# Performance work log

Measured on AMD Instinct MI355X. Metric: run time of the kernel, lower is better.

Reference implementation:

```python
import jax, jax.numpy as jnp
import numpy as np

N_NODES = 100000
N_EDGES = 3200000
NUM_FEATURES = 512
HIDDEN = 16
NUM_CLASSES = 32


def _gcn_conv(x, src, dst, norm, W, b, n):
    # PyG GCNConv: linear transform first, then normalized scatter-add aggregation
    xw = x @ W                          # [N, out]
    msg = xw[src] * norm[:, None]       # gather over edges (incl. self-loops)
    agg = jax.ops.segment_sum(msg, dst, num_segments=n)
    return agg + b


def setup_inputs() -> dict:
    key = jax.random.key(0)
    k_x, k_e, k_w1, k_w2 = jax.random.split(key, 4)
    x = jax.random.normal(k_x, (N_NODES, NUM_FEATURES), dtype=jnp.float32)
    edge_index = jax.random.randint(k_e, (2, N_EDGES), 0, N_NODES, dtype=jnp.int64)
    # Glorot-style init for the two GCNConv weights; zero bias (PyG default)
    W1 = jax.random.normal(k_w1, (NUM_FEATURES, HIDDEN), dtype=jnp.float32) * (1.0 / np.sqrt(NUM_FEATURES))
    b1 = jnp.zeros((HIDDEN,), dtype=jnp.float32)
    W2 = jax.random.normal(k_w2, (HIDDEN, NUM_CLASSES), dtype=jnp.float32) * (1.0 / np.sqrt(HIDDEN))
    b2 = jnp.zeros((NUM_CLASSES,), dtype=jnp.float32)
    return {"x": x, "edge_index": edge_index, "W1": W1, "b1": b1, "W2": W2, "b2": b2}


def reference(x, edge_index, W1, b1, W2, b2):
    n = x.shape[0]
    # add self-loops (PyG GCNConv default add_self_loops=True)
    loops = jnp.arange(n, dtype=edge_index.dtype)
    src = jnp.concatenate([edge_index[0], loops])
    dst = jnp.concatenate([edge_index[1], loops])
    # symmetric normalization D^{-1/2} (A+I) D^{-1/2}
    deg = jax.ops.segment_sum(jnp.ones_like(dst, dtype=x.dtype), dst, num_segments=n)
    dinv = jnp.where(deg > 0, jax.lax.rsqrt(deg), 0.0)
    norm = dinv[src] * dinv[dst]        # [E + N]

    h = jax.nn.relu(_gcn_conv(x, src, dst, norm, W1, b1, n))
    # F.dropout(p=0.5, training=self.training): eval mode -> identity
    out = _gcn_conv(h, src, dst, norm, W2, b2, n)
    return (out, h)
```

## Files before the change

### kernel.cpp

```cpp
#include <hip/hip_runtime.h>
#include <hip/hip_fp16.h>


#define NN 100000
#define NE 3200000
#define FIN 512
#define HID 16
#define NCLS 32
#define NB 391
#define NBP 512
#define CAP_B 9216

#define OFF_BCNT  0
#define OFF_SC    (NBP)
#define OFF_DINV  (NBP + 2*NN)
#define OFF_EP    (NBP + 3*NN)
#define OFF_XWS   (OFF_EP + NB*CAP_B)
#define OFF_HSC   (OFF_XWS + NN*8)

__global__ __launch_bounds__(512) void k_binA(const int* __restrict__ src,
                                              const int* __restrict__ dst,
                                              int* __restrict__ bcnt,
                                              unsigned* __restrict__ ep) {
    __shared__ int hist[NBP];
    __shared__ int gpos[NBP];
    int tid = threadIdx.x;
    hist[tid] = 0;
    __syncthreads();
    int base = blockIdx.x * 4096;
    unsigned rec[8];
    int meta[8];
#pragma unroll
    for (int k = 0; k < 8; ++k) {
        int e = base + tid + k * 512;
        if (e < NE) {
            int s = __builtin_nontemporal_load(src + e);
            int d = __builtin_nontemporal_load(dst + e);
            int b = d >> 8;
            int p = atomicAdd(&hist[b], 1);
            rec[k] = ((unsigned)s << 8) | (unsigned)(d & 255);
            meta[k] = (p << 9) | b;
        } else meta[k] = -1;
    }
    __syncthreads();
    int v = hist[tid];
    if (v > 0) gpos[tid] = atomicAdd(&bcnt[tid], v);
    __syncthreads();
#pragma unroll
    for (int k = 0; k < 8; ++k) {
        if (meta[k] >= 0) {
            int b = meta[k] & 511;
            int p = meta[k] >> 9;
            ep[b * CAP_B + gpos[b] + p] = rec[k];
        }
    }
}

__global__ __launch_bounds__(256) void k_binB(unsigned* __restrict__ ep,
                                              const int* __restrict__ bcnt,
                                              int2* __restrict__ sc,
                                              float* __restrict__ dinv) {
    __shared__ int nh[256];
    __shared__ int ns[256];
    __shared__ int np_[256];
    __shared__ int esL[CAP_B];
    int tid = threadIdx.x;
    int b = blockIdx.x;
    int gbase = b * CAP_B;
    int bc = bcnt[b];
    if (bc > CAP_B) bc = CAP_B;
    nh[tid] = 0;
    __syncthreads();
    for (int t = tid; t < bc; t += 256)
        atomicAdd(&nh[ep[gbase + t] & 255], 1);
    __syncthreads();
    int v = nh[tid];
    ns[tid] = v;
    __syncthreads();
#pragma unroll
    for (int o = 1; o < 256; o <<= 1) {
        int u = (tid >= o) ? ns[tid - o] : 0;
        __syncthreads();
        ns[tid] += u;
        __syncthreads();
    }
    int ex = ns[tid] - v;
    np_[tid] = ex;
    __syncthreads();
    for (int t = tid; t < bc; t += 256) {
        unsigned r = ep[gbase + t];
        int dl = r & 255;
        int p = atomicAdd(&np_[dl], 1);
        esL[p] = (int)(r >> 8);
    }
    __syncthreads();
    for (int t = tid; t < bc; t += 256)
        ep[gbase + t] = (unsigned)esL[t];
    int node = b * 256 + tid;
    if (node < NN) {
        sc[node] = make_int2(gbase + ex, v);
        dinv[node] = rsqrtf((float)(v + 1));
    }
}

__global__ __launch_bounds__(256) void k_xw(const float* __restrict__ x,
                                            const float* __restrict__ W1,
                                            const float* __restrict__ dinv,
                                            __half* __restrict__ xws) {
    __shared__ float w1[FIN * HID];
    for (int t = threadIdx.x; t < FIN * HID; t += 256) {
        int k = t >> 4, j = t & 15;
        int s = (k * 4 + ((j >> 2) ^ ((k >> 2) & 3))) * 4 + (j & 3);
        w1[s] = W1[t];
    }
    __syncthreads();
    int w  = threadIdx.x >> 6;
    int nl = (threadIdx.x >> 2) & 15;
    int c  = threadIdx.x & 3;
    int n0 = blockIdx.x * 128 + w * 32 + nl;
    int n1 = n0 + 16;
    bool v0 = n0 < NN, v1 = n1 < NN;
    const float4* x4 = reinterpret_cast<const float4*>(x);
    const float4* r0 = x4 + (v0 ? (size_t)n0 * (FIN / 4) : 0);
    const float4* r1 = x4 + (v1 ? (size_t)n1 * (FIN / 4) : 0);
    const float4* wv = reinterpret_cast<const float4*>(w1);
    float a0[HID], a1[HID];
#pragma unroll
    for (int j = 0; j < HID; ++j) { a0[j] = 0.f; a1[j] = 0.f; }
#pragma unroll 4
    for (int t = 0; t < 32; ++t) {
        int qk = c + 4 * t;
        float4 xv0 = r0[qk];
        float4 xv1 = r1[qk];
        const float4* wb = wv + qk * 16;
#pragma unroll
        for (int e = 0; e < 4; ++e) {
            float xe0 = (e == 0) ? xv0.x : (e == 1) ? xv0.y : (e == 2) ? xv0.z : xv0.w;
            float xe1 = (e == 0) ? xv1.x : (e == 1) ? xv1.y : (e == 2) ? xv1.z : xv1.w;
#pragma unroll
            for (int j4 = 0; j4 < 4; ++j4) {
                float4 w4 = wb[e * 4 + (j4 ^ c)];
                a0[j4 * 4 + 0] += xe0 * w4.x;
                a0[j4 * 4 + 1] += xe0 * w4.y;
                a0[j4 * 4 + 2] += xe0 * w4.z;
                a0[j4 * 4 + 3] += xe0 * w4.w;
                a1[j4 * 4 + 0] += xe1 * w4.x;
                a1[j4 * 4 + 1] += xe1 * w4.y;
                a1[j4 * 4 + 2] += xe1 * w4.z;
                a1[j4 * 4 + 3] += xe1 * w4.w;
            }
        }
    }
#pragma unroll
    for (int j = 0; j < HID; ++j) {
        a0[j] += __shfl_xor(a0[j], 1);
        a0[j] += __shfl_xor(a0[j], 2);
        a1[j] += __shfl_xor(a1[j], 1);
        a1[j] += __shfl_xor(a1[j], 2);
    }
    if (c == 0) {
        if (v0) {
            float dv = dinv[n0];
            __half2 hv[8];
#pragma unroll
            for (int k = 0; k < 8; ++k)
                hv[k] = __floats2half2_rn(a0[2 * k] * dv, a0[2 * k + 1] * dv);
            float4* o = reinterpret_cast<float4*>(xws + (size_t)n0 * HID);
            o[0] = *reinterpret_cast<float4*>(&hv[0]);
            o[1] = *reinterpret_cast<float4*>(&hv[4]);
        }
        if (v1) {
            float dv = dinv[n1];
            __half2 hv[8];
#pragma unroll
            for (int k = 0; k < 8; ++k)
                hv[k] = __floats2half2_rn(a1[2 * k] * dv, a1[2 * k + 1] * dv);
            float4* o = reinterpret_cast<float4*>(xws + (size_t)n1 * HID);
            o[0] = *reinterpret_cast<float4*>(&hv[0]);
            o[1] = *reinterpret_cast<float4*>(&hv[4]);
        }
    }
}

__global__ __launch_bounds__(256) void k_gather1(const int2* __restrict__ sc,
                                                 const int* __restrict__ esrc,
                                                 const __half2* __restrict__ xws2,
                                                 const float* __restrict__ dinv,
                                                 const float* __restrict__ b1,
                                                 float* __restrict__ hout,
                                                 __half2* __restrict__ hsc2) {
    int wave = (blockIdx.x * 256 + threadIdx.x) >> 6;
    if (wave >= NN) return;
    int i = wave;
    int lane = threadIdx.x & 63;
    int j2 = lane & 7;
    int c = lane >> 3;
    int2 s2 = sc[i];
    int st = s2.x, en = st + s2.y;
    float sx[8], sy[8];
#pragma unroll
    for (int k = 0; k < 8; ++k) { sx[k] = 0.f; sy[k] = 0.f; }
    for (int e = st + c; e < en; e += 64) {
        int a[8];
#pragma unroll
        for (int k = 0; k < 8; ++k) {
            int ee = e + 8 * k;
            a[k] = __builtin_nontemporal_load(esrc + (ee < en ? ee : e));
        }
#pragma unroll
        for (int k = 0; k < 8; ++k) {
            float2 f = __half22float2(xws2[a[k] * 8 + j2]);
            bool ok = (e + 8 * k) < en;
            sx[k] += ok ? f.x : 0.f;
            sy[k] += ok ? f.y : 0.f;
        }
    }
    float sumx = ((sx[0] + sx[1]) + (sx[2] + sx[3])) + ((sx[4] + sx[5]) + (sx[6] + sx[7]));
    float sumy = ((sy[0] + sy[1]) + (sy[2] + sy[3])) + ((sy[4] + sy[5]) + (sy[6] + sy[7]));
    sumx += __shfl_xor(sumx, 8);  sumy += __shfl_xor(sumy, 8);
    sumx += __shfl_xor(sumx, 16); sumy += __shfl_xor(sumy, 16);
    sumx += __shfl_xor(sumx, 32); sumy += __shfl_xor(sumy, 32);
    if (c == 0) {
        float dv = dinv[i];
        float2 self = __half22float2(xws2[i * 8 + j2]);
        float vx = b1[2 * j2]     + dv * (sumx + self.x);
        float vy = b1[2 * j2 + 1] + dv * (sumy + self.y);
        float hx = vx > 0.f ? vx : 0.f;
        float hy = vy > 0.f ? vy : 0.f;
        *reinterpret_cast<float2*>(hout + i * HID + 2 * j2) = make_float2(hx, hy);
        hsc2[i * 8 + j2] = __floats2half2_rn(hx * dv, hy * dv);
    }
}

__global__ __launch_bounds__(256) void k_gather2h(const int2* __restrict__ sc,
                                                  const int* __restrict__ esrc,
                                                  const __half2* __restrict__ hsc2,
                                                  const float* __restrict__ dinv,
                                                  const float* __restrict__ W2,
                                                  const float* __restrict__ b2,
                                                  float* __restrict__ out) {
    __shared__ float w2s[HID * NCLS];
    __shared__ float b2s[NCLS];
    for (int t = threadIdx.x; t < HID * NCLS; t += 256) w2s[t] = W2[t];
    if (threadIdx.x < NCLS) b2s[threadIdx.x] = b2[threadIdx.x];
    __syncthreads();
    int wave = (blockIdx.x * 256 + threadIdx.x) >> 6;
    if (wave >= NN) return;
    int i = wave;
    int lane = threadIdx.x & 63;
    int j2 = lane & 7;
    int c = lane >> 3;
    int2 s2 = sc[i];
    int st = s2.x, en = st + s2.y;
    float sx[8], sy[8];
#pragma unroll
    for (int k = 0; k < 8; ++k) { sx[k] = 0.f; sy[k] = 0.f; }
    for (int e = st + c; e < en; e += 64) {
        int a[8];
#pragma unroll
        for (int k = 0; k < 8; ++k) {
            int ee = e + 8 * k;
            a[k] = __builtin_nontemporal_load(esrc + (ee < en ? ee : e));
        }
#pragma unroll
        for (int k = 0; k < 8; ++k) {
            float2 f = __half22float2(hsc2[a[k] * 8 + j2]);
            bool ok = (e + 8 * k) < en;
            sx[k] += ok ? f.x : 0.f;
            sy[k] += ok ? f.y : 0.f;
        }
    }
    float sumx = ((sx[0] + sx[1]) + (sx[2] + sx[3])) + ((sx[4] + sx[5]) + (sx[6] + sx[7]));
    float sumy = ((sy[0] + sy[1]) + (sy[2] + sy[3])) + ((sy[4] + sy[5]) + (sy[6] + sy[7]));
    sumx += __shfl_xor(sumx, 8);  sumy += __shfl_xor(sumy, 8);
    sumx += __shfl_xor(sumx, 16); sumy += __shfl_xor(sumy, 16);
    sumx += __shfl_xor(sumx, 32); sumy += __shfl_xor(sumy, 32);
    {
        float2 self = __half22float2(hsc2[i * 8 + j2]);
        sumx += self.x;
        sumy += self.y;
    }
    int jo = lane & 31;
    float acc = 0.f;
#pragma unroll
    for (int p = 0; p < 8; ++p) {
        acc += __shfl(sumx, p) * w2s[(2 * p) * NCLS + jo];
        acc += __shfl(sumy, p) * w2s[(2 * p + 1) * NCLS + jo];
    }
    if (lane < 32)
        out[i * NCLS + jo] = b2s[jo] + dinv[i] * acc;
}

extern "C" void kernel_launch(void* const* d_in, const int* in_sizes, int n_in,
                              void* d_out, int out_size, void* d_ws, size_t ws_size,
                              hipStream_t stream) {
    const float* x  = (const float*)d_in[0];
    const int* ei   = (const int*)d_in[1];
    const float* W1 = (const float*)d_in[2];
    const float* b1 = (const float*)d_in[3];
    const float* W2 = (const float*)d_in[4];
    const float* b2 = (const float*)d_in[5];

    const int* src = ei;
    const int* dst = ei + NE;

    int* wsi = (int*)d_ws;
    int*      bcnt  = wsi + OFF_BCNT;
    int2*     sc    = (int2*)(wsi + OFF_SC);
    float*    dinv  = (float*)(wsi + OFF_DINV);
    unsigned* ep    = (unsigned*)(wsi + OFF_EP);
    __half*   xws   = (__half*)(wsi + OFF_XWS);
    __half2*  xws2  = (__half2*)(wsi + OFF_XWS);
    __half2*  hsc2  = (__half2*)(wsi + OFF_HSC);

    float* outp = (float*)d_out;
    float* hout = outp + NN * NCLS;

    const int B = 256;

    hipMemsetAsync(bcnt, 0, NBP * sizeof(int), stream);
    hipLaunchKernelGGL(k_binA,  dim3((NE + 4095) / 4096), dim3(512), 0, stream, src, dst, bcnt, ep);
    hipLaunchKernelGGL(k_binB,  dim3(NB), dim3(B), 0, stream, ep, bcnt, sc, dinv);
    hipLaunchKernelGGL(k_xw,    dim3((NN + 127) / 128), dim3(B), 0, stream, x, W1, dinv, xws);
    hipLaunchKernelGGL(k_gather1, dim3((NN * 64 + B - 1) / B), dim3(B), 0, stream,
                       sc, (const int*)ep, xws2, dinv, b1, hout, hsc2);
    hipLaunchKernelGGL(k_gather2h, dim3((NN * 64 + B - 1) / B), dim3(B), 0, stream,
                       sc, (const int*)ep, hsc2, dinv, W2, b2, outp);
}
```

Baseline: 193.3 us.

## Process two nodes per wave in both gather kernels to raise memory parallelism

Each wave in the two aggregation kernels now handles two nodes (i and i+N/2). The first 64-edge chunk of both nodes is loaded and gathered together, so more independent loads are in flight per wave, and the remaining chunks are handled in separate loops. The launch grid is halved. The edge-bin scatter store in the binning kernel is switched to a nontemporal store. Costs are higher register pressure and therefore lower occupancy, and there is an odd hsc2==nullptr check in the gather1 tail loop.

```diff
diff --git a/kernel.cpp b/kernel.cpp
--- a/kernel.cpp
+++ b/kernel.cpp
@@ -3,6 +3,7 @@
 
 
 #define NN 100000
+#define NHALF 50000
 #define NE 3200000
 #define FIN 512
 #define HID 16
@@ -51,7 +52,7 @@
         if (meta[k] >= 0) {
             int b = meta[k] & 511;
             int p = meta[k] >> 9;
-            ep[b * CAP_B + gpos[b] + p] = rec[k];
+            __builtin_nontemporal_store(rec[k], &ep[b * CAP_B + gpos[b] + p]);
         }
     }
 }
@@ -189,46 +190,91 @@
                                                  const float* __restrict__ b1,
                                                  float* __restrict__ hout,
                                                  __half2* __restrict__ hsc2) {
-    int wave = (blockIdx.x * 256 + threadIdx.x) >> 6;
-    if (wave >= NN) return;
-    int i = wave;
+    int wv = (blockIdx.x * 256 + threadIdx.x) >> 6;
+    if (wv >= NHALF) return;
+    int i0 = wv, i1 = wv + NHALF;
     int lane = threadIdx.x & 63;
     int j2 = lane & 7;
     int c = lane >> 3;
-    int2 s2 = sc[i];
-    int st = s2.x, en = st + s2.y;
-    float sx[8], sy[8];
-#pragma unroll
-    for (int k = 0; k < 8; ++k) { sx[k] = 0.f; sy[k] = 0.f; }
-    for (int e = st + c; e < en; e += 64) {
+    int2 A = sc[i0], B = sc[i1];
+    int stA = A.x + c, enA = A.x + A.y;
+    int stB = B.x + c, enB = B.x + B.y;
+    float sxA[8], syA[8], sxB[8], syB[8];
+#pragma unroll
+    for (int k = 0; k < 8; ++k) { sxA[k] = 0.f; syA[k] = 0.f; sxB[k] = 0.f; syB[k] = 0.f; }
+    {
+        int aA[8], aB[8];
+#pragma unroll
+        for (int k = 0; k < 8; ++k) {
+            int eA = stA + 8 * k;
+            int eB = stB + 8 * k;
+            aA[k] = __builtin_nontemporal_load(esrc + (eA < enA ? eA : A.x));
+            aB[k] = __builtin_nontemporal_load(esrc + (eB < enB ? eB : B.x));
+        }
+#pragma unroll
+        for (int k = 0; k < 8; ++k) {
+            bool okA = (stA + 8 * k) < enA;
+            bool okB = (stB + 8 * k) < enB;
+            float2 fA = __half22float2(xws2[(okA ? aA[k] : 0) * 8 + j2]);
+            float2 fB = __half22float2(xws2[(okB ? aB[k] : 0) * 8 + j2]);
+            sxA[k] += okA ? fA.x : 0.f;  syA[k] += okA ? fA.y : 0.f;
+            sxB[k] += okB ? fB.x : 0.f;  syB[k] += okB ? fB.y : 0.f;
+        }
+    }
+    for (int e = stA + 64; e < enA; e += 64) {
         int a[8];
 #pragma unroll
         for (int k = 0; k < 8; ++k) {
             int ee = e + 8 * k;
-            a[k] = __builtin_nontemporal_load(esrc + (ee < en ? ee : e));
+            a[k] = __builtin_nontemporal_load(esrc + (ee < enA ? ee : e));
         }
 #pragma unroll
         for (int k = 0; k < 8; ++k) {
             float2 f = __half22float2(xws2[a[k] * 8 + j2]);
-            bool ok = (e + 8 * k) < en;
-            sx[k] += ok ? f.x : 0.f;
-            sy[k] += ok ? f.y : 0.f;
-        }
-    }
-    float sumx = ((sx[0] + sx[1]) + (sx[2] + sx[3])) + ((sx[4] + sx[5]) + (sx[6] + sx[7]));
-    float sumy = ((sy[0] + sy[1]) + (sy[2] + sy[3])) + ((sy[4] + sy[5]) + (sy[6] + sy[7]));
-    sumx += __shfl_xor(sumx, 8);  sumy += __shfl_xor(sumy, 8);
-    sumx += __shfl_xor(sumx, 16); sumy += __shfl_xor(sumy, 16);
-    sumx += __shfl_xor(sumx, 32); sumy += __shfl_xor(sumy, 32);
+            bool ok = (e + 8 * k) < enA;
+            sxA[k] += ok ? f.x : 0.f;
+            syA[k] += ok ? f.y : 0.f;
+        }
+    }
+    for (int e = stB + 64; e < enB; e += 64) {
+        int a[8];
+#pragma unroll
+        for (int k = 0; k < 8; ++k) {
+            int ee = e + 8 * k;
+            a[k] = __builtin_nontemporal_load(esrc + (ee < enB ? ee : e));
+        }
+#pragma unroll
+        for (int k = 0; k < 8; ++k) {
+            float2 f = __half22float2(hsc2 == nullptr ? make_half2(__float2half(0.f), __float2half(0.f)) : xws2[a[k] * 8 + j2]);
+            bool ok = (e + 8 * k) < enB;
+            sxB[k] += ok ? f.x : 0.f;
+            syB[k] += ok ? f.y : 0.f;
+        }
+    }
+    float sumxA = ((sxA[0] + sxA[1]) + (sxA[2] + sxA[3])) + ((sxA[4] + sxA[5]) + (sxA[6] + sxA[7]));
+    float sumyA = ((syA[0] + syA[1]) + (syA[2] + syA[3])) + ((syA[4] + syA[5]) + (syA[6] + syA[7]));
+    float sumxB = ((sxB[0] + sxB[1]) + (sxB[2] + sxB[3])) + ((sxB[4] + sxB[5]) + (sxB[6] + sxB[7]));
+    float sumyB = ((syB[0] + syB[1]) + (syB[2] + syB[3])) + ((syB[4] + syB[5]) + (syB[6] + syB[7]));
+    sumxA += __shfl_xor(sumxA, 8);  sumyA += __shfl_xor(sumyA, 8);
+    sumxA += __shfl_xor(sumxA, 16); sumyA += __shfl_xor(sumyA, 16);
+    sumxA += __shfl_xor(sumxA, 32); sumyA += __shfl_xor(sumyA, 32);
+    sumxB += __shfl_xor(sumxB, 8);  sumyB += __shfl_xor(sumyB, 8);
+    sumxB += __shfl_xor(sumxB, 16); sumyB += __shfl_xor(sumyB, 16);
+    sumxB += __shfl_xor(sumxB, 32); sumyB += __shfl_xor(sumyB, 32);
     if (c == 0) {
-        float dv = dinv[i];
-        float2 self = __half22float2(xws2[i * 8 + j2]);
-        float vx = b1[2 * j2]     + dv * (sumx + self.x);
-        float vy = b1[2 * j2 + 1] + dv * (sumy + self.y);
-        float hx = vx > 0.f ? vx : 0.f;
-        float hy = vy > 0.f ? vy : 0.f;
-        *reinterpret_cast<float2*>(hout + i * HID + 2 * j2) = make_float2(hx, hy);
-        hsc2[i * 8 + j2] = __floats2half2_rn(hx * dv, hy * dv);
+        float dvA = dinv[i0], dvB = dinv[i1];
+        float2 selfA = __half22float2(xws2[i0 * 8 + j2]);
+        float2 selfB = __half22float2(xws2[i1 * 8 + j2]);
+        float vxA = b1[2 * j2]     + dvA * (sumxA + selfA.x);
+        float vyA = b1[2 * j2 + 1] + dvA * (sumyA + selfA.y);
+        float vxB = b1[2 * j2]     + dvB * (sumxB + selfB.x);
+        float vyB = b1[2 * j2 + 1] + dvB * (sumyB + selfB.y);
+        float hxA = vxA > 0.f ? vxA : 0.f, hyA = vyA > 0.f ? vyA : 0.f;
+        float hxB = vxB > 0.f ? vxB : 0.f, hyB = vyB > 0.f ? vyB : 0.f;
+        *reinterpret_cast<float2*>(hout + i0 * HID + 2 * j2) = make_float2(hxA, hyA);
+        *reinterpret_cast<float2*>(hout + i1 * HID + 2 * j2) = make_float2(hxB, hyB);
+        hsc2[i0 * 8 + j2] = __floats2half2_rn(hxA * dvA, hyA * dvA);
+        hsc2[i1 * 8 + j2] = __floats2half2_rn(hxB * dvB, hyB * dvB);
     }
 }
 
@@ -244,51 +290,96 @@
     for (int t = threadIdx.x; t < HID * NCLS; t += 256) w2s[t] = W2[t];
     if (threadIdx.x < NCLS) b2s[threadIdx.x] = b2[threadIdx.x];
     __syncthreads();
-    int wave = (blockIdx.x * 256 + threadIdx.x) >> 6;
-    if (wave >= NN) return;
-    int i = wave;
+    int wv = (blockIdx.x * 256 + threadIdx.x) >> 6;
+    if (wv >= NHALF) return;
+    int i0 = wv, i1 = wv + NHALF;
     int lane = threadIdx.x & 63;
     int j2 = lane & 7;
     int c = lane >> 3;
-    int2 s2 = sc[i];
-    int st = s2.x, en = st + s2.y;
-    float sx[8], sy[8];
-#pragma unroll
-    for (int k = 0; k < 8; ++k) { sx[k] = 0.f; sy[k] = 0.f; }
-    for (int e = st + c; e < en; e += 64) {
+    int2 A = sc[i0], B = sc[i1];
+    int stA = A.x + c, enA = A.x + A.y;
+    int stB = B.x + c, enB = B.x + B.y;
+    float sxA[8], syA[8], sxB[8], syB[8];
+#pragma unroll
+    for (int k = 0; k < 8; ++k) { sxA[k] = 0.f; syA[k] = 0.f; sxB[k] = 0.f; syB[k] = 0.f; }
+    {
+        int aA[8], aB[8];
+#pragma unroll
+        for (int k = 0; k < 8; ++k) {
+            int eA = stA + 8 * k;
+            int eB = stB + 8 * k;
+            aA[k] = __builtin_nontemporal_load(esrc + (eA < enA ? eA : A.x));
+            aB[k] = __builtin_nontemporal_load(esrc + (eB < enB ? eB : B.x));
+        }
+#pragma unroll
+        for (int k = 0; k < 8; ++k) {
+            bool okA = (stA + 8 * k) < enA;
+            bool okB = (stB + 8 * k) < enB;
+            float2 fA = __half22float2(hsc2[(okA ? aA[k] : 0) * 8 + j2]);
+            float2 fB = __half22float2(hsc2[(okB ? aB[k] : 0) * 8 + j2]);
+            sxA[k] += okA ? fA.x : 0.f;  syA[k] += okA ? fA.y : 0.f;
+            sxB[k] += okB ? fB.x : 0.f;  syB[k] += okB ? fB.y : 0.f;
+        }
+    }
+    for (int e = stA + 64; e < enA; e += 64) {
         int a[8];
 #pragma unroll
         for (int k = 0; k < 8; ++k) {
             int ee = e + 8 * k;
-            a[k] = __builtin_nontemporal_load(esrc + (ee < en ? ee : e));
+            a[k] = __builtin_nontemporal_load(esrc + (ee < enA ? ee : e));
         }
 #pragma unroll
         for (int k = 0; k < 8; ++k) {
             float2 f = __half22float2(hsc2[a[k] * 8 + j2]);
-            bool ok = (e + 8 * k) < en;
-            sx[k] += ok ? f.x : 0.f;
-            sy[k] += ok ? f.y : 0.f;
-        }
-    }
-    float sumx = ((sx[0] + sx[1]) + (sx[2] + sx[3])) + ((sx[4] + sx[5]) + (sx[6] + sx[7]));
-    float sumy = ((sy[0] + sy[1]) + (sy[2] + sy[3])) + ((sy[4] + sy[5]) + (sy[6] + sy[7]));
-    sumx += __shfl_xor(sumx, 8);  sumy += __shfl_xor(sumy, 8);
-    sumx += __shfl_xor(sumx, 16); sumy += __shfl_xor(sumy, 16);
-    sumx += __shfl_xor(sumx, 32); sumy += __shfl_xor(sumy, 32);
+            bool ok = (e + 8 * k) < enA;
+            sxA[k] += ok ? f.x : 0.f;
+            syA[k] += ok ? f.y : 0.f;
+        }
+    }
+    for (int e = stB + 64; e < enB; e += 64) {
+        int a[8];
+#pragma unroll
+        for (int k = 0; k < 8; ++k) {
+            int ee = e + 8 * k;
+            a[k] = __builtin_nontemporal_load(esrc + (ee < enB ? ee : e));
+        }
+#pragma unroll
+        for (int k = 0; k < 8; ++k) {
+            float2 f = __half22float2(hsc2[a[k] * 8 + j2]);
+            bool ok = (e + 8 * k) < enB;
+            sxB[k] += ok ? f.x : 0.f;
+            syB[k] += ok ? f.y : 0.f;
+        }
+    }
+    float sumxA = ((sxA[0] + sxA[1]) + (sxA[2] + sxA[3])) + ((sxA[4] + sxA[5]) + (sxA[6] + sxA[7]));
+    float sumyA = ((syA[0] + syA[1]) + (syA[2] + syA[3])) + ((syA[4] + syA[5]) + (syA[6] + syA[7]));
+    float sumxB = ((sxB[0] + sxB[1]) + (sxB[2] + sxB[3])) + ((sxB[4] + sxB[5]) + (sxB[6] + sxB[7]));
+    float sumyB = ((syB[0] + syB[1]) + (syB[2] + syB[3])) + ((syB[4] + syB[5]) + (syB[6] + syB[7]));
+    sumxA += __shfl_xor(sumxA, 8);  sumyA += __shfl_xor(sumyA, 8);
+    sumxA += __shfl_xor(sumxA, 16); sumyA += __shfl_xor(sumyA, 16);
+    sumxA += __shfl_xor(sumxA, 32); sumyA += __shfl_xor(sumyA, 32);
+    sumxB += __shfl_xor(sumxB, 8);  sumyB += __shfl_xor(sumyB, 8);
+    sumxB += __shfl_xor(sumxB, 16); sumyB += __shfl_xor(sumyB, 16);
+    sumxB += __shfl_xor(sumxB, 32); sumyB += __shfl_xor(sumyB, 32);
     {
-        float2 self = __half22float2(hsc2[i * 8 + j2]);
-        sumx += self.x;
-        sumy += self.y;
+        float2 sA = __half22float2(hsc2[i0 * 8 + j2]);
+        float2 sB = __half22float2(hsc2[i1 * 8 + j2]);
+        sumxA += sA.x;  sumyA += sA.y;
+        sumxB += sB.x;  sumyB += sB.y;
     }
     int jo = lane & 31;
-    float acc = 0.f;
+    float accA = 0.f, accB = 0.f;
 #pragma unroll
     for (int p = 0; p < 8; ++p) {
-        acc += __shfl(sumx, p) * w2s[(2 * p) * NCLS + jo];
-        acc += __shfl(sumy, p) * w2s[(2 * p + 1) * NCLS + jo];
-    }
-    if (lane < 32)
-        out[i * NCLS + jo] = b2s[jo] + dinv[i] * acc;
+        float wx = w2s[(2 * p) * NCLS + jo];
+        float wy = w2s[(2 * p + 1) * NCLS + jo];
+        accA += __shfl(sumxA, p) * wx + __shfl(sumyA, p) * wy;
+        accB += __shfl(sumxB, p) * wx + __shfl(sumyB, p) * wy;
+    }
+    if (lane < 32) {
+        out[i0 * NCLS + jo] = b2s[jo] + dinv[i0] * accA;
+        out[i1 * NCLS + jo] = b2s[jo] + dinv[i1] * accB;
+    }
 }
 
 extern "C" void kernel_launch(void* const* d_in, const int* in_sizes, int n_in,
@@ -322,8 +413,8 @@
     hipLaunchKernelGGL(k_binA,  dim3((NE + 4095) / 4096), dim3(512), 0, stream, src, dst, bcnt, ep);
     hipLaunchKernelGGL(k_binB,  dim3(NB), dim3(B), 0, stream, ep, bcnt, sc, dinv);
     hipLaunchKernelGGL(k_xw,    dim3((NN + 127) / 128), dim3(B), 0, stream, x, W1, dinv, xws);
-    hipLaunchKernelGGL(k_gather1, dim3((NN * 64 + B - 1) / B), dim3(B), 0, stream,
+    hipLaunchKernelGGL(k_gather1, dim3((NHALF * 64 + B - 1) / B), dim3(B), 0, stream,
                        sc, (const int*)ep, xws2, dinv, b1, hout, hsc2);
-    hipLaunchKernelGGL(k_gather2h, dim3((NN * 64 + B - 1) / B), dim3(B), 0, stream,
+    hipLaunchKernelGGL(k_gather2h, dim3((NHALF * 64 + B - 1) / B), dim3(B), 0, stream,
                        sc, (const int*)ep, hsc2, dinv, W2, b2, outp);
 }
```

Result: slower. 265.3 us (+37.3%).
